# Performance work log

Hardware: AMD Instinct MI355X
Metric: run time of the kernel (lower is better)

The kernel has to match this reference:

```python
import jax, jax.numpy as jnp
import numpy as np

N_HEAD = 16
MASK_NEG = 1e10  # matches torch's -10000000000.0 * (1 - b)


def setup_inputs() -> dict:
    key = jax.random.key(0)
    ks = jax.random.split(key, 9)
    B, S, D = 2, 2048, 2048
    std = 0.02
    inp = {
        "x": jax.random.normal(ks[0], (B, S, D), dtype=jnp.float32),
        "Wq": jax.random.normal(ks[1], (D, D), dtype=jnp.float32) * std,
        "bq": jnp.zeros((D,), dtype=jnp.float32),
        "Wk": jax.random.normal(ks[2], (D, D), dtype=jnp.float32) * std,
        "bk": jnp.zeros((D,), dtype=jnp.float32),
        "Wv": jax.random.normal(ks[3], (D, D), dtype=jnp.float32) * std,
        "bv": jnp.zeros((D,), dtype=jnp.float32),
        "Wd": jax.random.normal(ks[4], (D, D), dtype=jnp.float32) * std,
        "bd": jnp.zeros((D,), dtype=jnp.float32),
    }
    return inp


def reference(x, Wq, bq, Wk, bk, Wv, bv, Wd, bd):
    # x: [B, S, D]; layer_past=None, query=None path (full causal prefill)
    B, S, D = x.shape
    H = N_HEAD
    hd = D // H

    def split(h):  # [B,S,D] -> [B,H,S,hd]
        return h.reshape(B, S, H, hd).transpose(0, 2, 1, 3)

    q = split(x @ Wq + bq)
    k = split(x @ Wk + bk)
    v = split(x @ Wv + bv)

    # scores [B,H,S,S]; scale=True divides by sqrt(head_dim)
    w = jnp.einsum("bhqd,bhkd->bhqk", q, k) / jnp.sqrt(jnp.float32(hd))
    b = jnp.tril(jnp.ones((S, S), dtype=w.dtype))  # causal bias buffer slice
    w = w * b - MASK_NEG * (1.0 - b)
    w = jax.nn.softmax(w, axis=-1)
    a = jnp.einsum("bhqk,bhkd->bhqd", w, v)

    a = a.transpose(0, 2, 1, 3).reshape(B, S, D)  # merge_heads
    a = a @ Wd + bd
    present = jnp.stack((k, v))  # [2, B, H, S, hd]
    return a, present
```

## Files before the change

kernel.cpp:

```cpp
#include <hip/hip_runtime.h>


typedef unsigned short ushort_t;
typedef __attribute__((ext_vector_type(8))) short short8;
typedef __attribute__((ext_vector_type(4))) float f32x4;

#define MFMA16x16x32 __builtin_amdgcn_mfma_f32_16x16x32_bf16
#define S_LEN   2048
#define DMODEL  2048
#define A_ELEMS 8388608
#define W_ELEMS 4194304

__device__ __forceinline__ ushort_t f2bf(float x) {
  unsigned u = __float_as_uint(x);
  u += 0x7FFFu + ((u >> 16) & 1u);
  return (ushort_t)(u >> 16);
}
__device__ __forceinline__ unsigned pack2(float lo, float hi) {
  return (unsigned)f2bf(lo) | ((unsigned)f2bf(hi) << 16);
}
struct f8 { float v[8]; };
__device__ __forceinline__ f8 ld8f(const float* p) {
  f8 r;
  float4 a = *(const float4*)p, b = *(const float4*)(p + 4);
  r.v[0]=a.x; r.v[1]=a.y; r.v[2]=a.z; r.v[3]=a.w;
  r.v[4]=b.x; r.v[5]=b.y; r.v[6]=b.z; r.v[7]=b.w;
  return r;
}
__device__ __forceinline__ uint4 cvt8(const f8& f) {
  uint4 o;
  o.x = pack2(f.v[0], f.v[1]); o.y = pack2(f.v[2], f.v[3]);
  o.z = pack2(f.v[4], f.v[5]); o.w = pack2(f.v[6], f.v[7]);
  return o;
}

typedef const __attribute__((address_space(1))) void* gas_t;
typedef __attribute__((address_space(3))) void* las_t;
__device__ __forceinline__ void gld16(const void* g, void* l) {
  __builtin_amdgcn_global_load_lds((gas_t)(unsigned long long)g,
                                   (las_t)(unsigned)(unsigned long long)l,
                                   16, 0, 0);
}

__global__ void __launch_bounds__(256) conv_x(const float* __restrict__ x,
                                              ushort_t* __restrict__ xb) {
  const int i = (blockIdx.x * 256 + threadIdx.x) * 8;
  f8 v = ld8f(x + i);
  *(uint4*)&xb[i] = cvt8(v);
}

__global__ void __launch_bounds__(256) trans_w(
    const float* __restrict__ w0, const float* __restrict__ w1,
    const float* __restrict__ w2, const float* __restrict__ w3,
    ushort_t* __restrict__ o0, ushort_t* __restrict__ o1,
    ushort_t* __restrict__ o2, ushort_t* __restrict__ o3) {
  __shared__ float t[64][65];
  const float* src; ushort_t* dst;
  switch (blockIdx.z) {
    case 0: src = w0; dst = o0; break;
    case 1: src = w1; dst = o1; break;
    case 2: src = w2; dst = o2; break;
    default: src = w3; dst = o3; break;
  }
  const int kb = blockIdx.y * 64, nb = blockIdx.x * 64;
  const int r = threadIdx.x >> 3, c8 = (threadIdx.x & 7) * 8;
#pragma unroll
  for (int i = 0; i < 64; i += 32) {
    *(float4*)&t[r + i][c8]     = *(const float4*)&src[(size_t)(kb + r + i) * DMODEL + nb + c8];
    *(float4*)&t[r + i][c8 + 4] = *(const float4*)&src[(size_t)(kb + r + i) * DMODEL + nb + c8 + 4];
  }
  __syncthreads();
#pragma unroll
  for (int i = 0; i < 64; i += 32) {
    float tmp[8];
#pragma unroll
    for (int j = 0; j < 8; ++j) tmp[j] = t[c8 + j][r + i];
    uint4 o;
    o.x = pack2(tmp[0], tmp[1]); o.y = pack2(tmp[2], tmp[3]);
    o.z = pack2(tmp[4], tmp[5]); o.w = pack2(tmp[6], tmp[7]);
    *(uint4*)&dst[(size_t)(nb + r + i) * DMODEL + kb + c8] = o;
  }
}

__global__ void __launch_bounds__(256) trans_v(const float* __restrict__ v,
                                               ushort_t* __restrict__ vt) {
  __shared__ float t[64][65];
  const int bh = blockIdx.z;
  const int sb = blockIdx.x * 64, db = blockIdx.y * 64;
  const float* src = v + (size_t)bh * S_LEN * 128;
  ushort_t* dst = vt + (size_t)bh * 128 * S_LEN;
  const int r = threadIdx.x >> 3, c8 = (threadIdx.x & 7) * 8;
#pragma unroll
  for (int i = 0; i < 64; i += 32) {
    *(float4*)&t[r + i][c8]     = *(const float4*)&src[(size_t)(sb + r + i) * 128 + db + c8];
    *(float4*)&t[r + i][c8 + 4] = *(const float4*)&src[(size_t)(sb + r + i) * 128 + db + c8 + 4];
  }
  __syncthreads();
#pragma unroll
  for (int i = 0; i < 64; i += 32) {
    float tmp[8];
#pragma unroll
    for (int j = 0; j < 8; ++j) tmp[j] = t[c8 + j][r + i];
    uint4 o;
    o.x = pack2(tmp[0], tmp[1]); o.y = pack2(tmp[2], tmp[3]);
    o.z = pack2(tmp[4], tmp[5]); o.w = pack2(tmp[6], tmp[7]);
    *(uint4*)&dst[(size_t)(db + r + i) * S_LEN + sb + c8] = o;
  }
}

#define ABUF (2 * 128 * 32)
#define BBUF (2 * 256 * 32)

__device__ __forceinline__ void stage6(
    const ushort_t* __restrict__ gA, const ushort_t* __restrict__ gB,
    ushort_t* An, ushort_t* Bn, int t, int w, size_t soff) {
  const size_t kc = (size_t)t * 64;
#pragma unroll
  for (int i = 0; i < 2; ++i) {
    const int c = 2 * w + i, kh = c >> 3, rg = c & 7;
    gld16(gA + (size_t)(rg * 16) * 2048 + kc + kh * 32 + soff,
          An + (kh * 128 + rg * 16) * 32);
  }
#pragma unroll
  for (int i = 0; i < 4; ++i) {
    const int c = 4 * w + i, kh = c >> 4, rg = c & 15;
    gld16(gB + (size_t)(rg * 16) * 2048 + kc + kh * 32 + soff,
          Bn + (kh * 256 + rg * 16) * 32);
  }
}

__device__ __forceinline__ void gemm2p_core(
    const ushort_t* __restrict__ gA, const ushort_t* __restrict__ gB,
    ushort_t* AsF, ushort_t* BsF, int w, int lane, f32x4 acc[4][4]) {
  const int l15 = lane & 15, quad = lane >> 4;
  const int wm = w >> 2, wn = w & 3;
  const size_t soff = (size_t)(lane >> 2) * 2048 +
                      (((lane & 3) ^ ((lane >> 3) & 3)) * 8);
  const int rslot8 = (quad ^ ((l15 >> 1) & 3)) * 8;
  const int arow = wm * 64 + l15;
  const int brow = wn * 64 + l15;

  stage6(gA, gB, AsF, BsF, 0, w, soff);
  __syncthreads();

  for (int t = 0; t < 32; ++t) {
    ushort_t* Ab = AsF + (t & 1) * ABUF;
    ushort_t* Bb = BsF + (t & 1) * BBUF;
    if (t + 1 < 32)
      stage6(gA, gB, AsF + ((t + 1) & 1) * ABUF, BsF + ((t + 1) & 1) * BBUF,
             t + 1, w, soff);
#pragma unroll
    for (int kh = 0; kh < 2; ++kh) {
      short8 af[4], bf[4];
#pragma unroll
      for (int mi = 0; mi < 4; ++mi)
        af[mi] = *(const short8*)&Ab[(kh * 128 + arow + mi * 16) * 32 + rslot8];
#pragma unroll
      for (int ni = 0; ni < 4; ++ni)
        bf[ni] = *(const short8*)&Bb[(kh * 256 + brow + ni * 16) * 32 + rslot8];
      __builtin_amdgcn_s_setprio(1);
#pragma unroll
      for (int mi = 0; mi < 4; ++mi)
#pragma unroll
        for (int ni = 0; ni < 4; ++ni)
          acc[mi][ni] = MFMA16x16x32(af[mi], bf[ni], acc[mi][ni], 0, 0, 0);
      __builtin_amdgcn_s_setprio(0);
    }
    __syncthreads();
  }
}

__global__ void __launch_bounds__(512, 2) gemm_qkv(
    const ushort_t* __restrict__ xb,
    const ushort_t* __restrict__ wtq, const ushort_t* __restrict__ wtk,
    const ushort_t* __restrict__ wtv,
    const float* __restrict__ bq, const float* __restrict__ bk,
    const float* __restrict__ bv,
    ushort_t* __restrict__ qout, float* __restrict__ kout,
    float* __restrict__ vout, ushort_t* __restrict__ kb16) {
  __shared__ ushort_t As_[2 * ABUF];
  __shared__ ushort_t Bs_[2 * BBUF];
  const int tid = threadIdx.x, w = tid >> 6, lane = tid & 63;
  const int l15 = lane & 15, quad = lane >> 4;
  const int wm = w >> 2, wn = w & 3;
  const int bx = blockIdx.x;
  const int logical = (bx & 7) * 96 + (bx >> 3);
  const int wid = logical >> 8, idx = logical & 255;
  const int tn = idx & 7, tm = idx >> 3;
  const ushort_t* Wt = wid == 0 ? wtq : (wid == 1 ? wtk : wtv);
  const float* bias = wid == 0 ? bq : (wid == 1 ? bk : bv);

  f32x4 acc[4][4] = {};
  gemm2p_core(xb + (size_t)(tm * 128) * 2048, Wt + (size_t)(tn * 256) * 2048,
              As_, Bs_, w, lane, acc);

  const int row0 = tm * 128 + wm * 64, col0 = tn * 256 + wn * 64;
#pragma unroll
  for (int ni = 0; ni < 4; ++ni) {
    const int col = col0 + ni * 16 + l15;
    const float bv_ = bias[col];
    const int h = col >> 7, d = col & 127;
#pragma unroll
    for (int mi = 0; mi < 4; ++mi) {
#pragma unroll
      for (int j = 0; j < 4; ++j) {
        const int row = row0 + mi * 16 + quad * 4 + j;
        const int b = row >> 11, s = row & 2047;
        const size_t idxg = (size_t)(((b * 16 + h) * 2048 + s)) * 128 + d;
        const float v = acc[mi][ni][j] + bv_;
        if (wid == 0) qout[idxg] = f2bf(v);
        else if (wid == 1) { kout[idxg] = v; kb16[idxg] = f2bf(v); }
        else vout[idxg] = v;
      }
    }
  }
}

__global__ void __launch_bounds__(512, 2) gemm_proj(
    const ushort_t* __restrict__ A, const ushort_t* __restrict__ Wt,
    const float* __restrict__ bias, float* __restrict__ C) {
  __shared__ ushort_t As_[2 * ABUF];
  __shared__ ushort_t Bs_[2 * BBUF];
  const int tid = threadIdx.x, w = tid >> 6, lane = tid & 63;
  const int l15 = lane & 15, quad = lane >> 4;
  const int wm = w >> 2, wn = w & 3;
  const int logical = (blockIdx.x & 7) * 32 + (blockIdx.x >> 3);
  const int tn = logical & 7, tm = logical >> 3;

  f32x4 acc[4][4] = {};
  gemm2p_core(A + (size_t)(tm * 128) * 2048, Wt + (size_t)(tn * 256) * 2048,
              As_, Bs_, w, lane, acc);

  const int row0 = tm * 128 + wm * 64, col0 = tn * 256 + wn * 64;
#pragma unroll
  for (int ni = 0; ni < 4; ++ni) {
    const int col = col0 + ni * 16 + l15;
    const float bv_ = bias[col];
#pragma unroll
    for (int mi = 0; mi < 4; ++mi)
#pragma unroll
      for (int j = 0; j < 4; ++j) {
        const int row = row0 + mi * 16 + quad * 4 + j;
        C[(size_t)row * DMODEL + col] = acc[mi][ni][j] + bv_;
      }
  }
}

__global__ void __launch_bounds__(512, 2) attn_fwd(
    const ushort_t* __restrict__ Q, const ushort_t* __restrict__ Kb,
    const ushort_t* __restrict__ Vt, ushort_t* __restrict__ O) {
  __shared__ ushort_t KP[128 * 136];
  __shared__ ushort_t Vs[128 * 128];
  const int tid = threadIdx.x;
  const int w = tid >> 6, lane = tid & 63;
  const int l15 = lane & 15, quad = lane >> 4;
  const int x7 = l15 & 7;
  const int bh = blockIdx.x & 31, pr = blockIdx.x >> 5;
  const int b = bh >> 4, h = bh & 15;
  const size_t base  = (size_t)bh * (S_LEN * 128);
  const size_t vbase = (size_t)bh * (128 * S_LEN);
  const float cs = 0.08838834764831845f * 1.4426950408889634f;

  const int srow = lane >> 4;
  const int schunk = lane & 15;

  for (int seg = 0; seg < 2; ++seg) {
    const int qt = (seg == 0) ? (15 - pr) : pr;
    const int q0 = qt * 128 + w * 16;

    short8 qf[4];
#pragma unroll
    for (int ks = 0; ks < 4; ++ks)
      qf[ks] = *(const short8*)&Q[base + (size_t)(q0 + l15) * 128 + ks * 32 + quad * 8];

    f32x4 oacc[8] = {};
    float mrun[4], lrun[4];
#pragma unroll
    for (int j = 0; j < 4; ++j) { mrun[j] = -1e30f; lrun[j] = 0.f; }

    for (int kt = 0; kt <= qt; ++kt) {
      const int kb_ = kt * 128;
      __syncthreads();
#pragma unroll
      for (int i = 0; i < 4; ++i) {
        const int r = w * 16 + i * 4 + srow;
        const int c = schunk ^ (r & 7);
        gld16(Kb + base + (size_t)(kb_ + r) * 128 + c * 8,
              (void*)(KP + (w * 16 + i * 4) * 128));
        gld16(Vt + vbase + (size_t)r * S_LEN + kb_ + c * 8,
              (void*)(Vs + (w * 16 + i * 4) * 128));
      }
      __syncthreads();

      f32x4 sacc[8] = {};
#pragma unroll
      for (int ks = 0; ks < 4; ++ks) {
        const int sw = ((ks * 4 + quad) ^ x7) * 8;
        short8 kf[8];
#pragma unroll
        for (int ni = 0; ni < 8; ++ni)
          kf[ni] = *(const short8*)&KP[(ni * 16 + l15) * 128 + sw];
#pragma unroll
        for (int ni = 0; ni < 8; ++ni)
          sacc[ni] = MFMA16x16x32(qf[ks], kf[ni], sacc[ni], 0, 0, 0);
      }
      __syncthreads();

#pragma unroll
      for (int j = 0; j < 4; ++j) {
        const int rl = quad * 4 + j;
        const int rowg = q0 + rl;
        float t0[8];
#pragma unroll
        for (int ni = 0; ni < 8; ++ni) {
          const int kg = kb_ + ni * 16 + l15;
          const float s = sacc[ni][j] * cs;
          t0[ni] = (kg <= rowg) ? s : -1e30f;
        }
        float rm = fmaxf(fmaxf(fmaxf(t0[0], t0[1]), fmaxf(t0[2], t0[3])),
                         fmaxf(fmaxf(t0[4], t0[5]), fmaxf(t0[6], t0[7])));
        rm = fmaxf(rm, __shfl_xor(rm, 1));
        rm = fmaxf(rm, __shfl_xor(rm, 2));
        rm = fmaxf(rm, __shfl_xor(rm, 4));
        rm = fmaxf(rm, __shfl_xor(rm, 8));
        const float mold = mrun[j];
        const float mnew = fmaxf(mold, rm);
        const float alpha = __builtin_amdgcn_exp2f(mold - mnew);
        float rs = 0.f;
#pragma unroll
        for (int ni = 0; ni < 8; ++ni) {
          const float pe = __builtin_amdgcn_exp2f(t0[ni] - mnew);
          rs += pe;
          KP[(w * 16 + rl) * 136 + ni * 16 + l15] = f2bf(pe);
        }
        rs += __shfl_xor(rs, 1);
        rs += __shfl_xor(rs, 2);
        rs += __shfl_xor(rs, 4);
        rs += __shfl_xor(rs, 8);
        lrun[j] = lrun[j] * alpha + rs;
        mrun[j] = mnew;
#pragma unroll
        for (int oi = 0; oi < 8; ++oi) oacc[oi][j] *= alpha;
      }

#pragma unroll
      for (int ks = 0; ks < 4; ++ks) {
        const int sw = ((ks * 4 + quad) ^ x7) * 8;
        short8 pf = *(const short8*)&KP[(w * 16 + l15) * 136 + ks * 32 + quad * 8];
        short8 vf[8];
#pragma unroll
        for (int oi = 0; oi < 8; ++oi)
          vf[oi] = *(const short8*)&Vs[(oi * 16 + l15) * 128 + sw];
#pragma unroll
        for (int oi = 0; oi < 8; ++oi)
          oacc[oi] = MFMA16x16x32(pf, vf[oi], oacc[oi], 0, 0, 0);
      }
    }

    {
      float inv[4];
#pragma unroll
      for (int j = 0; j < 4; ++j) inv[j] = 1.f / lrun[j];
#pragma unroll
      for (int oi = 0; oi < 8; ++oi) {
        const int oc = oi * 16 + l15;
#pragma unroll
        for (int j = 0; j < 4; ++j) {
          const int s = q0 + quad * 4 + j;
          O[((size_t)(b * S_LEN + s)) * DMODEL + h * 128 + oc] =
              f2bf(oacc[oi][j] * inv[j]);
        }
      }
    }
  }
}

extern "C" void kernel_launch(void* const* d_in, const int* in_sizes, int n_in,
                              void* d_out, int out_size, void* d_ws,
                              size_t ws_size, hipStream_t stream) {
  const float* x  = (const float*)d_in[0];
  const float* Wq = (const float*)d_in[1];
  const float* bq = (const float*)d_in[2];
  const float* Wk = (const float*)d_in[3];
  const float* bk = (const float*)d_in[4];
  const float* Wv = (const float*)d_in[5];
  const float* bv = (const float*)d_in[6];
  const float* Wd = (const float*)d_in[7];
  const float* bd = (const float*)d_in[8];

  float* out   = (float*)d_out;
  float* a_out = out;
  float* k_out = out + A_ELEMS;
  float* v_out = out + 2 * A_ELEMS;
  ushort_t* ob  = (ushort_t*)d_out;
  ushort_t* xb   = ob;
  ushort_t* q_ws = ob + A_ELEMS;

  ushort_t* ws  = (ushort_t*)d_ws;
  ushort_t* wtq = ws;
  ushort_t* wtk = ws + W_ELEMS;
  ushort_t* wtv = ws + 2 * (size_t)W_ELEMS;
  ushort_t* wtd = ws + 3 * (size_t)W_ELEMS;
  ushort_t* attn_ws = ws + 4 * (size_t)W_ELEMS;
  ushort_t* kb_ws   = attn_ws + (size_t)A_ELEMS;
  ushort_t* vt_ws   = attn_ws + 2 * (size_t)A_ELEMS;

  conv_x<<<4096, 256, 0, stream>>>(x, xb);
  trans_w<<<dim3(32, 32, 4), 256, 0, stream>>>(Wq, Wk, Wv, Wd,
                                               wtq, wtk, wtv, wtd);
  gemm_qkv<<<768, 512, 0, stream>>>(xb, wtq, wtk, wtv, bq, bk, bv,
                                    q_ws, k_out, v_out, kb_ws);
  trans_v<<<dim3(32, 2, 32), 256, 0, stream>>>(v_out, vt_ws);
  attn_fwd<<<256, 512, 0, stream>>>(q_ws, kb_ws, vt_ws, attn_ws);
  gemm_proj<<<256, 512, 0, stream>>>(attn_ws, wtd, bd, a_out);
}
```

Measured before the change: 446.6 us.

## Enlarge GEMM tiles to 256x256 with 8-phase interleaved load/MFMA pipeline

The QKV and output-projection GEMMs move from 128x256 tiles to 256x256 tiles, with each wave computing a 128x64 sub-tile (8x4 accumulators). The main loop is split into four phases, each issuing a half-tile global-to-LDS load between LDS fragment reads and MFMA bursts, with explicit vmcnt waits and raw barriers. The aim is more data reuse per LDS byte and better overlap of memory traffic with matrix math. In exchange it uses more registers and 128KB of LDS per block, which may lower occupancy, and it halves the grid to 384 and 128 blocks, which may underfill the 256 CUs.

New measurement: 475.5 us. 1.06x slower.

```diff
diff --git a/kernel.cpp b/kernel.cpp
--- a/kernel.cpp
+++ b/kernel.cpp
@@ -108,65 +108,129 @@
   }
 }
 
-#define ABUF (2 * 128 * 32)
-#define BBUF (2 * 256 * 32)
-
-__device__ __forceinline__ void stage6(
+__device__ __forceinline__ void stage_half(
+    const ushort_t* __restrict__ g,
+    ushort_t* lds_half,
+    int t, int kh, int w, int lane) {
+  const size_t soff = (size_t)(lane >> 2) * 2048 +
+                      (((lane & 3) ^ ((lane >> 3) & 3)) << 3);
+  const size_t kc = (size_t)(t * 64 + kh * 32);
+#pragma unroll
+  for (int i = 0; i < 2; ++i) {
+    const int wc = i * 8 + w;
+    gld16(g + (size_t)(wc * 16) * 2048 + kc + soff,
+          (void*)(lds_half + wc * 512));
+  }
+}
+
+__device__ __forceinline__ void gemm8p_core(
     const ushort_t* __restrict__ gA, const ushort_t* __restrict__ gB,
-    ushort_t* An, ushort_t* Bn, int t, int w, size_t soff) {
-  const size_t kc = (size_t)t * 64;
-#pragma unroll
-  for (int i = 0; i < 2; ++i) {
-    const int c = 2 * w + i, kh = c >> 3, rg = c & 7;
-    gld16(gA + (size_t)(rg * 16) * 2048 + kc + kh * 32 + soff,
-          An + (kh * 128 + rg * 16) * 32);
-  }
-#pragma unroll
-  for (int i = 0; i < 4; ++i) {
-    const int c = 4 * w + i, kh = c >> 4, rg = c & 15;
-    gld16(gB + (size_t)(rg * 16) * 2048 + kc + kh * 32 + soff,
-          Bn + (kh * 256 + rg * 16) * 32);
-  }
-}
-
-__device__ __forceinline__ void gemm2p_core(
-    const ushort_t* __restrict__ gA, const ushort_t* __restrict__ gB,
-    ushort_t* AsF, ushort_t* BsF, int w, int lane, f32x4 acc[4][4]) {
+    ushort_t* As_, ushort_t* Bs_, int w, int lane, f32x4 acc[8][4]) {
   const int l15 = lane & 15, quad = lane >> 4;
   const int wm = w >> 2, wn = w & 3;
-  const size_t soff = (size_t)(lane >> 2) * 2048 +
-                      (((lane & 3) ^ ((lane >> 3) & 3)) * 8);
-  const int rslot8 = (quad ^ ((l15 >> 1) & 3)) * 8;
-  const int arow = wm * 64 + l15;
-  const int brow = wn * 64 + l15;
-
-  stage6(gA, gB, AsF, BsF, 0, w, soff);
-  __syncthreads();
-
-  for (int t = 0; t < 32; ++t) {
-    ushort_t* Ab = AsF + (t & 1) * ABUF;
-    ushort_t* Bb = BsF + (t & 1) * BBUF;
-    if (t + 1 < 32)
-      stage6(gA, gB, AsF + ((t + 1) & 1) * ABUF, BsF + ((t + 1) & 1) * BBUF,
-             t + 1, w, soff);
+  const int rs8 = (quad ^ ((l15 >> 1) & 3)) << 3;
+  const int arow0 = wm * 128 + l15;
+  const int brow0 = wn * 64 + l15;
+
+  stage_half(gA, As_,                0, 0, w, lane);
+  stage_half(gB, Bs_,                0, 0, w, lane);
+  stage_half(gA, As_ + 8192,         0, 1, w, lane);
+  stage_half(gB, Bs_ + 8192,         0, 1, w, lane);
+  stage_half(gA, As_ + 16384,        1, 0, w, lane);
+  stage_half(gB, Bs_ + 16384,        1, 0, w, lane);
+  asm volatile("s_waitcnt vmcnt(8)" ::: "memory");
+  asm volatile("s_barrier" ::: "memory");
+
+  short8 af[4], bf[4];
+  for (int t = 0; t < 31; ++t) {
+    const int cb = t & 1, nb = (t + 1) & 1;
+    ushort_t* Ab = As_ + cb * 16384;
+    ushort_t* Bb = Bs_ + cb * 16384;
+#pragma unroll
+    for (int mi = 0; mi < 4; ++mi)
+      af[mi] = *(const short8*)&Ab[(arow0 + mi * 16) * 32 + rs8];
+#pragma unroll
+    for (int ni = 0; ni < 4; ++ni)
+      bf[ni] = *(const short8*)&Bb[(brow0 + ni * 16) * 32 + rs8];
+    stage_half(gA, As_ + nb * 16384 + 8192, t + 1, 1, w, lane);
+    asm volatile("s_barrier" ::: "memory");
+    __builtin_amdgcn_s_setprio(1);
+#pragma unroll
+    for (int mi = 0; mi < 4; ++mi)
+#pragma unroll
+      for (int ni = 0; ni < 4; ++ni)
+        acc[mi][ni] = MFMA16x16x32(af[mi], bf[ni], acc[mi][ni], 0, 0, 0);
+    __builtin_amdgcn_s_setprio(0);
+    asm volatile("s_barrier" ::: "memory");
+#pragma unroll
+    for (int mi = 0; mi < 4; ++mi)
+      af[mi] = *(const short8*)&Ab[(arow0 + 64 + mi * 16) * 32 + rs8];
+    stage_half(gB, Bs_ + nb * 16384 + 8192, t + 1, 1, w, lane);
+    asm volatile("s_barrier" ::: "memory");
+    __builtin_amdgcn_s_setprio(1);
+#pragma unroll
+    for (int mi = 0; mi < 4; ++mi)
+#pragma unroll
+      for (int ni = 0; ni < 4; ++ni)
+        acc[4 + mi][ni] = MFMA16x16x32(af[mi], bf[ni], acc[4 + mi][ni], 0, 0, 0);
+    __builtin_amdgcn_s_setprio(0);
+    asm volatile("s_waitcnt vmcnt(8)" ::: "memory");
+    asm volatile("s_barrier" ::: "memory");
+#pragma unroll
+    for (int mi = 0; mi < 4; ++mi)
+      af[mi] = *(const short8*)&Ab[8192 + (arow0 + mi * 16) * 32 + rs8];
+#pragma unroll
+    for (int ni = 0; ni < 4; ++ni)
+      bf[ni] = *(const short8*)&Bb[8192 + (brow0 + ni * 16) * 32 + rs8];
+    if (t + 2 < 32) stage_half(gA, As_ + cb * 16384, t + 2, 0, w, lane);
+    asm volatile("s_barrier" ::: "memory");
+    __builtin_amdgcn_s_setprio(1);
+#pragma unroll
+    for (int mi = 0; mi < 4; ++mi)
+#pragma unroll
+      for (int ni = 0; ni < 4; ++ni)
+        acc[mi][ni] = MFMA16x16x32(af[mi], bf[ni], acc[mi][ni], 0, 0, 0);
+    __builtin_amdgcn_s_setprio(0);
+    asm volatile("s_barrier" ::: "memory");
+#pragma unroll
+    for (int mi = 0; mi < 4; ++mi)
+      af[mi] = *(const short8*)&Ab[8192 + (arow0 + 64 + mi * 16) * 32 + rs8];
+    if (t + 2 < 32) stage_half(gB, Bs_ + cb * 16384, t + 2, 0, w, lane);
+    asm volatile("s_barrier" ::: "memory");
+    __builtin_amdgcn_s_setprio(1);
+#pragma unroll
+    for (int mi = 0; mi < 4; ++mi)
+#pragma unroll
+      for (int ni = 0; ni < 4; ++ni)
+        acc[4 + mi][ni] = MFMA16x16x32(af[mi], bf[ni], acc[4 + mi][ni], 0, 0, 0);
+    __builtin_amdgcn_s_setprio(0);
+    asm volatile("s_waitcnt vmcnt(8)" ::: "memory");
+    asm volatile("s_barrier" ::: "memory");
+  }
+  asm volatile("s_waitcnt vmcnt(0)" ::: "memory");
+  asm volatile("s_barrier" ::: "memory");
+  {
+    ushort_t* Ab = As_ + 16384;
+    ushort_t* Bb = Bs_ + 16384;
 #pragma unroll
     for (int kh = 0; kh < 2; ++kh) {
-      short8 af[4], bf[4];
-#pragma unroll
-      for (int mi = 0; mi < 4; ++mi)
-        af[mi] = *(const short8*)&Ab[(kh * 128 + arow + mi * 16) * 32 + rslot8];
 #pragma unroll
       for (int ni = 0; ni < 4; ++ni)
-        bf[ni] = *(const short8*)&Bb[(kh * 256 + brow + ni * 16) * 32 + rslot8];
-      __builtin_amdgcn_s_setprio(1);
-#pragma unroll
-      for (int mi = 0; mi < 4; ++mi)
-#pragma unroll
-        for (int ni = 0; ni < 4; ++ni)
-          acc[mi][ni] = MFMA16x16x32(af[mi], bf[ni], acc[mi][ni], 0, 0, 0);
-      __builtin_amdgcn_s_setprio(0);
+        bf[ni] = *(const short8*)&Bb[kh * 8192 + (brow0 + ni * 16) * 32 + rs8];
+#pragma unroll
+      for (int mh = 0; mh < 2; ++mh) {
+#pragma unroll
+        for (int mi = 0; mi < 4; ++mi)
+          af[mi] = *(const short8*)&Ab[kh * 8192 +
+                                       (arow0 + mh * 64 + mi * 16) * 32 + rs8];
+#pragma unroll
+        for (int mi = 0; mi < 4; ++mi)
+#pragma unroll
+          for (int ni = 0; ni < 4; ++ni)
+            acc[mh * 4 + mi][ni] =
+                MFMA16x16x32(af[mi], bf[ni], acc[mh * 4 + mi][ni], 0, 0, 0);
+      }
     }
-    __syncthreads();
   }
 }
 
@@ -178,39 +242,41 @@
     const float* __restrict__ bv,
     ushort_t* __restrict__ qout, float* __restrict__ kout,
     float* __restrict__ vout, ushort_t* __restrict__ kb16) {
-  __shared__ ushort_t As_[2 * ABUF];
-  __shared__ ushort_t Bs_[2 * BBUF];
+  __shared__ ushort_t As_[32768];
+  __shared__ ushort_t Bs_[32768];
   const int tid = threadIdx.x, w = tid >> 6, lane = tid & 63;
   const int l15 = lane & 15, quad = lane >> 4;
   const int wm = w >> 2, wn = w & 3;
-  const int bx = blockIdx.x;
-  const int logical = (bx & 7) * 96 + (bx >> 3);
-  const int wid = logical >> 8, idx = logical & 255;
-  const int tn = idx & 7, tm = idx >> 3;
+  const int logical = (blockIdx.x & 7) * 48 + (blockIdx.x >> 3);
+  const int wid = logical >> 7, r = logical & 127;
+  const int tn = r & 7, tm = r >> 3;
   const ushort_t* Wt = wid == 0 ? wtq : (wid == 1 ? wtk : wtv);
   const float* bias = wid == 0 ? bq : (wid == 1 ? bk : bv);
 
-  f32x4 acc[4][4] = {};
-  gemm2p_core(xb + (size_t)(tm * 128) * 2048, Wt + (size_t)(tn * 256) * 2048,
+  f32x4 acc[8][4] = {};
+  gemm8p_core(xb + (size_t)(tm * 256) * 2048, Wt + (size_t)(tn * 256) * 2048,
               As_, Bs_, w, lane, acc);
 
-  const int row0 = tm * 128 + wm * 64, col0 = tn * 256 + wn * 64;
+  const int row0 = tm * 256 + wm * 128, col0 = tn * 256 + wn * 64;
 #pragma unroll
   for (int ni = 0; ni < 4; ++ni) {
     const int col = col0 + ni * 16 + l15;
     const float bv_ = bias[col];
     const int h = col >> 7, d = col & 127;
 #pragma unroll
-    for (int mi = 0; mi < 4; ++mi) {
-#pragma unroll
-      for (int j = 0; j < 4; ++j) {
-        const int row = row0 + mi * 16 + quad * 4 + j;
-        const int b = row >> 11, s = row & 2047;
-        const size_t idxg = (size_t)(((b * 16 + h) * 2048 + s)) * 128 + d;
-        const float v = acc[mi][ni][j] + bv_;
-        if (wid == 0) qout[idxg] = f2bf(v);
-        else if (wid == 1) { kout[idxg] = v; kb16[idxg] = f2bf(v); }
-        else vout[idxg] = v;
+    for (int mh = 0; mh < 2; ++mh) {
+#pragma unroll
+      for (int mi = 0; mi < 4; ++mi) {
+#pragma unroll
+        for (int j = 0; j < 4; ++j) {
+          const int row = row0 + mh * 64 + mi * 16 + quad * 4 + j;
+          const int b = row >> 11, s = row & 2047;
+          const size_t idxg = (size_t)(((b * 16 + h) * 2048 + s)) * 128 + d;
+          const float v = acc[mh * 4 + mi][ni][j] + bv_;
+          if (wid == 0) qout[idxg] = f2bf(v);
+          else if (wid == 1) { kout[idxg] = v; kb16[idxg] = f2bf(v); }
+          else vout[idxg] = v;
+        }
       }
     }
   }
@@ -219,30 +285,32 @@
 __global__ void __launch_bounds__(512, 2) gemm_proj(
     const ushort_t* __restrict__ A, const ushort_t* __restrict__ Wt,
     const float* __restrict__ bias, float* __restrict__ C) {
-  __shared__ ushort_t As_[2 * ABUF];
-  __shared__ ushort_t Bs_[2 * BBUF];
+  __shared__ ushort_t As_[32768];
+  __shared__ ushort_t Bs_[32768];
   const int tid = threadIdx.x, w = tid >> 6, lane = tid & 63;
   const int l15 = lane & 15, quad = lane >> 4;
   const int wm = w >> 2, wn = w & 3;
-  const int logical = (blockIdx.x & 7) * 32 + (blockIdx.x >> 3);
+  const int logical = (blockIdx.x & 7) * 16 + (blockIdx.x >> 3);
   const int tn = logical & 7, tm = logical >> 3;
 
-  f32x4 acc[4][4] = {};
-  gemm2p_core(A + (size_t)(tm * 128) * 2048, Wt + (size_t)(tn * 256) * 2048,
+  f32x4 acc[8][4] = {};
+  gemm8p_core(A + (size_t)(tm * 256) * 2048, Wt + (size_t)(tn * 256) * 2048,
               As_, Bs_, w, lane, acc);
 
-  const int row0 = tm * 128 + wm * 64, col0 = tn * 256 + wn * 64;
+  const int row0 = tm * 256 + wm * 128, col0 = tn * 256 + wn * 64;
 #pragma unroll
   for (int ni = 0; ni < 4; ++ni) {
     const int col = col0 + ni * 16 + l15;
     const float bv_ = bias[col];
 #pragma unroll
-    for (int mi = 0; mi < 4; ++mi)
-#pragma unroll
-      for (int j = 0; j < 4; ++j) {
-        const int row = row0 + mi * 16 + quad * 4 + j;
-        C[(size_t)row * DMODEL + col] = acc[mi][ni][j] + bv_;
-      }
+    for (int mh = 0; mh < 2; ++mh)
+#pragma unroll
+      for (int mi = 0; mi < 4; ++mi)
+#pragma unroll
+        for (int j = 0; j < 4; ++j) {
+          const int row = row0 + mh * 64 + mi * 16 + quad * 4 + j;
+          C[(size_t)row * DMODEL + col] = acc[mh * 4 + mi][ni][j] + bv_;
+        }
   }
 }
 
@@ -408,9 +476,9 @@
   conv_x<<<4096, 256, 0, stream>>>(x, xb);
   trans_w<<<dim3(32, 32, 4), 256, 0, stream>>>(Wq, Wk, Wv, Wd,
                                                wtq, wtk, wtv, wtd);
-  gemm_qkv<<<768, 512, 0, stream>>>(xb, wtq, wtk, wtv, bq, bk, bv,
+  gemm_qkv<<<384, 512, 0, stream>>>(xb, wtq, wtk, wtv, bq, bk, bv,
                                     q_ws, k_out, v_out, kb_ws);
   trans_v<<<dim3(32, 2, 32), 256, 0, stream>>>(v_out, vt_ws);
   attn_fwd<<<256, 512, 0, stream>>>(q_ws, kb_ws, vt_ws, attn_ws);
-  gemm_proj<<<256, 512, 0, stream>>>(attn_ws, wtd, bd, a_out);
-}
+  gemm_proj<<<128, 512, 0, stream>>>(attn_ws, wtd, bd, a_out);
+}
```

## Split attention into one q-tile per block with 4 waves of 32 rows

Applied to the files above, without the earlier changes.

The attention kernel now launches 512 blocks of 256 threads, each handling a single 128-row query tile, instead of 256 blocks of 512 threads that each processed two paired tiles sequentially. Each wave now owns 32 query rows (two 16-row MFMA tiles), so every K/V fragment read from LDS feeds twice as many MFMAs. The aim is more blocks for scheduling and less LDS traffic per MFMA. The cost is more registers per wave and a loss of the explicit causal load balancing from pairing short and long tiles, which is left to the hardware scheduler.

New measurement: 507.9 us. +13.7%, slower.

```diff
diff --git a/kernel.cpp b/kernel.cpp
--- a/kernel.cpp
+++ b/kernel.cpp
@@ -246,7 +246,7 @@
   }
 }
 
-__global__ void __launch_bounds__(512, 2) attn_fwd(
+__global__ void __launch_bounds__(256, 2) attn_fwd(
     const ushort_t* __restrict__ Q, const ushort_t* __restrict__ Kb,
     const ushort_t* __restrict__ Vt, ushort_t* __restrict__ O) {
   __shared__ ushort_t KP[128 * 136];
@@ -255,7 +255,8 @@
   const int w = tid >> 6, lane = tid & 63;
   const int l15 = lane & 15, quad = lane >> 4;
   const int x7 = l15 & 7;
-  const int bh = blockIdx.x & 31, pr = blockIdx.x >> 5;
+  const int bh = blockIdx.x & 31, t16 = blockIdx.x >> 5;
+  const int qt = (t16 < 8) ? (15 - t16) : (t16 - 8);
   const int b = bh >> 4, h = bh & 15;
   const size_t base  = (size_t)bh * (S_LEN * 128);
   const size_t vbase = (size_t)bh * (128 * S_LEN);
@@ -264,57 +265,64 @@
   const int srow = lane >> 4;
   const int schunk = lane & 15;
 
-  for (int seg = 0; seg < 2; ++seg) {
-    const int qt = (seg == 0) ? (15 - pr) : pr;
-    const int q0 = qt * 128 + w * 16;
-
-    short8 qf[4];
+  const int q0 = qt * 128 + w * 32;
+
+  short8 qf[2][4];
+#pragma unroll
+  for (int mi = 0; mi < 2; ++mi)
 #pragma unroll
     for (int ks = 0; ks < 4; ++ks)
-      qf[ks] = *(const short8*)&Q[base + (size_t)(q0 + l15) * 128 + ks * 32 + quad * 8];
-
-    f32x4 oacc[8] = {};
-    float mrun[4], lrun[4];
-#pragma unroll
-    for (int j = 0; j < 4; ++j) { mrun[j] = -1e30f; lrun[j] = 0.f; }
-
-    for (int kt = 0; kt <= qt; ++kt) {
-      const int kb_ = kt * 128;
-      __syncthreads();
-#pragma unroll
-      for (int i = 0; i < 4; ++i) {
-        const int r = w * 16 + i * 4 + srow;
-        const int c = schunk ^ (r & 7);
-        gld16(Kb + base + (size_t)(kb_ + r) * 128 + c * 8,
-              (void*)(KP + (w * 16 + i * 4) * 128));
-        gld16(Vt + vbase + (size_t)r * S_LEN + kb_ + c * 8,
-              (void*)(Vs + (w * 16 + i * 4) * 128));
-      }
-      __syncthreads();
-
-      f32x4 sacc[8] = {};
-#pragma unroll
-      for (int ks = 0; ks < 4; ++ks) {
-        const int sw = ((ks * 4 + quad) ^ x7) * 8;
-        short8 kf[8];
+      qf[mi][ks] = *(const short8*)&Q[base +
+          (size_t)(q0 + mi * 16 + l15) * 128 + ks * 32 + quad * 8];
+
+  f32x4 oacc[2][8] = {};
+  float mrun[2][4], lrun[2][4];
+#pragma unroll
+  for (int mi = 0; mi < 2; ++mi)
+#pragma unroll
+    for (int j = 0; j < 4; ++j) { mrun[mi][j] = -1e30f; lrun[mi][j] = 0.f; }
+
+  for (int kt = 0; kt <= qt; ++kt) {
+    const int kb_ = kt * 128;
+    __syncthreads();
+#pragma unroll
+    for (int i = 0; i < 8; ++i) {
+      const int r = w * 32 + i * 4 + srow;
+      const int c = schunk ^ (r & 7);
+      gld16(Kb + base + (size_t)(kb_ + r) * 128 + c * 8,
+            (void*)(KP + (w * 32 + i * 4) * 128));
+      gld16(Vt + vbase + (size_t)r * S_LEN + kb_ + c * 8,
+            (void*)(Vs + (w * 32 + i * 4) * 128));
+    }
+    __syncthreads();
+
+    f32x4 sacc[2][8] = {};
+#pragma unroll
+    for (int ks = 0; ks < 4; ++ks) {
+      const int sw = ((ks * 4 + quad) ^ x7) * 8;
+      short8 kf[8];
+#pragma unroll
+      for (int ni = 0; ni < 8; ++ni)
+        kf[ni] = *(const short8*)&KP[(ni * 16 + l15) * 128 + sw];
+#pragma unroll
+      for (int mi = 0; mi < 2; ++mi)
 #pragma unroll
         for (int ni = 0; ni < 8; ++ni)
-          kf[ni] = *(const short8*)&KP[(ni * 16 + l15) * 128 + sw];
-#pragma unroll
-        for (int ni = 0; ni < 8; ++ni)
-          sacc[ni] = MFMA16x16x32(qf[ks], kf[ni], sacc[ni], 0, 0, 0);
-      }
-      __syncthreads();
-
+          sacc[mi][ni] = MFMA16x16x32(qf[mi][ks], kf[ni], sacc[mi][ni], 0, 0, 0);
+    }
+    __syncthreads();
+
+#pragma unroll
+    for (int mi = 0; mi < 2; ++mi) {
 #pragma unroll
       for (int j = 0; j < 4; ++j) {
-        const int rl = quad * 4 + j;
+        const int rl = mi * 16 + quad * 4 + j;
         const int rowg = q0 + rl;
         float t0[8];
 #pragma unroll
         for (int ni = 0; ni < 8; ++ni) {
           const int kg = kb_ + ni * 16 + l15;
-          const float s = sacc[ni][j] * cs;
+          const float s = sacc[mi][ni][j] * cs;
           t0[ni] = (kg <= rowg) ? s : -1e30f;
         }
         float rm = fmaxf(fmaxf(fmaxf(t0[0], t0[1]), fmaxf(t0[2], t0[3])),
@@ -323,7 +331,7 @@
         rm = fmaxf(rm, __shfl_xor(rm, 2));
         rm = fmaxf(rm, __shfl_xor(rm, 4));
         rm = fmaxf(rm, __shfl_xor(rm, 8));
-        const float mold = mrun[j];
+        const float mold = mrun[mi][j];
         const float mnew = fmaxf(mold, rm);
         const float alpha = __builtin_amdgcn_exp2f(mold - mnew);
         float rs = 0.f;
@@ -331,45 +339,51 @@
         for (int ni = 0; ni < 8; ++ni) {
           const float pe = __builtin_amdgcn_exp2f(t0[ni] - mnew);
           rs += pe;
-          KP[(w * 16 + rl) * 136 + ni * 16 + l15] = f2bf(pe);
+          KP[(w * 32 + rl) * 136 + ni * 16 + l15] = f2bf(pe);
         }
         rs += __shfl_xor(rs, 1);
         rs += __shfl_xor(rs, 2);
         rs += __shfl_xor(rs, 4);
         rs += __shfl_xor(rs, 8);
-        lrun[j] = lrun[j] * alpha + rs;
-        mrun[j] = mnew;
-#pragma unroll
-        for (int oi = 0; oi < 8; ++oi) oacc[oi][j] *= alpha;
+        lrun[mi][j] = lrun[mi][j] * alpha + rs;
+        mrun[mi][j] = mnew;
+#pragma unroll
+        for (int oi = 0; oi < 8; ++oi) oacc[mi][oi][j] *= alpha;
       }
-
-#pragma unroll
-      for (int ks = 0; ks < 4; ++ks) {
-        const int sw = ((ks * 4 + quad) ^ x7) * 8;
-        short8 pf = *(const short8*)&KP[(w * 16 + l15) * 136 + ks * 32 + quad * 8];
-        short8 vf[8];
+    }
+
+#pragma unroll
+    for (int ks = 0; ks < 4; ++ks) {
+      const int sw = ((ks * 4 + quad) ^ x7) * 8;
+      short8 pf[2], vf[8];
+#pragma unroll
+      for (int mi = 0; mi < 2; ++mi)
+        pf[mi] = *(const short8*)&KP[(w * 32 + mi * 16 + l15) * 136 +
+                                     ks * 32 + quad * 8];
+#pragma unroll
+      for (int oi = 0; oi < 8; ++oi)
+        vf[oi] = *(const short8*)&Vs[(oi * 16 + l15) * 128 + sw];
+#pragma unroll
+      for (int mi = 0; mi < 2; ++mi)
 #pragma unroll
         for (int oi = 0; oi < 8; ++oi)
-          vf[oi] = *(const short8*)&Vs[(oi * 16 + l15) * 128 + sw];
-#pragma unroll
-        for (int oi = 0; oi < 8; ++oi)
-          oacc[oi] = MFMA16x16x32(pf, vf[oi], oacc[oi], 0, 0, 0);
-      }
-    }
-
-    {
-      float inv[4];
-#pragma unroll
-      for (int j = 0; j < 4; ++j) inv[j] = 1.f / lrun[j];
-#pragma unroll
-      for (int oi = 0; oi < 8; ++oi) {
-        const int oc = oi * 16 + l15;
-#pragma unroll
-        for (int j = 0; j < 4; ++j) {
-          const int s = q0 + quad * 4 + j;
-          O[((size_t)(b * S_LEN + s)) * DMODEL + h * 128 + oc] =
-              f2bf(oacc[oi][j] * inv[j]);
-        }
+          oacc[mi][oi] = MFMA16x16x32(pf[mi], vf[oi], oacc[mi][oi], 0, 0, 0);
+    }
+  }
+
+#pragma unroll
+  for (int mi = 0; mi < 2; ++mi) {
+    float inv[4];
+#pragma unroll
+    for (int j = 0; j < 4; ++j) inv[j] = 1.f / lrun[mi][j];
+#pragma unroll
+    for (int oi = 0; oi < 8; ++oi) {
+      const int oc = oi * 16 + l15;
+#pragma unroll
+      for (int j = 0; j < 4; ++j) {
+        const int s = q0 + mi * 16 + quad * 4 + j;
+        O[((size_t)(b * S_LEN + s)) * DMODEL + h * 128 + oc] =
+            f2bf(oacc[mi][oi][j] * inv[j]);
       }
     }
   }
@@ -411,6 +425,6 @@
   gemm_qkv<<<768, 512, 0, stream>>>(xb, wtq, wtk, wtv, bq, bk, bv,
                                     q_ws, k_out, v_out, kb_ws);
   trans_v<<<dim3(32, 2, 32), 256, 0, stream>>>(v_out, vt_ws);
-  attn_fwd<<<256, 512, 0, stream>>>(q_ws, kb_ws, vt_ws, attn_ws);
+  attn_fwd<<<512, 256, 0, stream>>>(q_ws, kb_ws, vt_ws, attn_ws);
   gemm_proj<<<256, 512, 0, stream>>>(attn_ws, wtd, bd, a_out);
 }
```
